# Kernel optimization log

Hardware: AMD Instinct MI355X
Metric: run time of the kernel (lower is better)

Reference implementation:

```python
import jax, jax.numpy as jnp
import numpy as np

H = 8          # heads
V = 25         # num_nodes
C_IN = 64      # node_channel_in
C_OUT = 64     # node_channel_out
M_IN = 64      # node_memory_in
N, T = 32, 256 # batch, time (t must equal mt)
DIN = V * C_IN     # 1600
DMEM = V * M_IN    # 1600
DOUT = V * C_OUT   # 1600


def setup_inputs() -> dict:
    key = jax.random.key(0)
    ks = jax.random.split(key, 8)
    s_in = 1.0 / np.sqrt(DIN)
    s_mem = 1.0 / np.sqrt(DMEM)
    return {
        "x": jax.random.normal(ks[0], (N, C_IN, T, V), jnp.float32),
        "m": jax.random.normal(ks[1], (N, M_IN, T, V), jnp.float32),
        # stacked per-head Linear weights, stored as [h, in, out]
        "Wk": jax.random.uniform(ks[2], (H, DIN, DOUT), jnp.float32, -s_in, s_in),
        "bk": jax.random.uniform(ks[3], (H, DOUT), jnp.float32, -s_in, s_in),
        "Wq": jax.random.uniform(ks[4], (H, DMEM, DOUT), jnp.float32, -s_mem, s_mem),
        "bq": jax.random.uniform(ks[5], (H, DOUT), jnp.float32, -s_mem, s_mem),
        "Wv": jax.random.uniform(ks[6], (H, DMEM, DOUT), jnp.float32, -s_mem, s_mem),
        "bv": jax.random.uniform(ks[7], (H, DOUT), jnp.float32, -s_mem, s_mem),
    }


def reference(x, m, Wk, bk, Wq, bq, Wv, bv):
    n, c, t, v = x.shape
    # [n,c,t,v] -> [n,t,c*v]
    xf = jnp.transpose(x, (0, 2, 1, 3)).reshape(n, t, c * v)
    mn, mc, mt, mv = m.shape
    mf = jnp.transpose(m, (0, 2, 1, 3)).reshape(mn, mt, mc * mv)
    # batched per-head projections: [n,h,t,dout]
    keys = jnp.einsum('ntf,hfo->nhto', xf, Wk) + bk[None, :, None, :]
    queries = jnp.einsum('ntf,hfo->nhto', mf, Wq) + bq[None, :, None, :]
    values = jnp.einsum('ntf,hfo->nhto', mf, Wv) + bv[None, :, None, :]
    scale = 1.0 / np.sqrt(C_OUT * V).astype(np.float32)
    # att: [n,h,mt,t]
    att = jnp.einsum('nhqd,nhkd->nhqk', queries, keys) * scale
    # NOTE: original applies softmax over dim=1 (the HEADS axis)
    att = jax.nn.softmax(att, axis=1)
    # [n,h,mt,t] @ [n,h,t(=mt),dout] -> [n,h,t,dout]
    y = jnp.einsum('nhqk,nhkd->nhqd', att, values)
    # [n,h,t,v*out] -> [n,t,v*out,h] -> [n,t,v,out*h] -> [n,out*h,t,v]
    y = jnp.transpose(y, (0, 2, 3, 1)).reshape(n, t, V, C_OUT * H)
    return jnp.transpose(y, (0, 3, 1, 2))
```

## Files before the change

### kernel.cpp

```cpp
#include <hip/hip_runtime.h>
#include <hip/hip_bf16.h>
#include <cstdint>

typedef __hip_bfloat16 bf16;
typedef __attribute__((ext_vector_type(8))) short short8;
typedef __attribute__((ext_vector_type(4))) float floatx4;

#define AS1 __attribute__((address_space(1)))
#define AS3 __attribute__((address_space(3)))

__device__ __forceinline__ int imin(int a, int b) { return a < b ? a : b; }

__device__ __forceinline__ void async_copy16(const void* g, void* l) {
  __builtin_amdgcn_global_load_lds((const AS1 uint32_t*)g, (AS3 uint32_t*)l, 16, 0, 0);
}

__global__ __launch_bounds__(256) void transpose_w(const float* __restrict__ W,
                                                   bf16* __restrict__ Wt) {
  __shared__ float tile[64][65];
  const float* Wh = W + (size_t)blockIdx.z * 2560000;
  bf16* Wth = Wt + (size_t)blockIdx.z * 2560000;
  const int i0 = blockIdx.x * 64;
  const int o0 = blockIdx.y * 64;
  for (int e = threadIdx.x; e < 4096; e += 256) {
    int r = e >> 6, c = e & 63;
    tile[r][c] = Wh[(size_t)(i0 + r) * 1600 + o0 + c];
  }
  __syncthreads();
  for (int e = threadIdx.x; e < 4096; e += 256) {
    int r = e >> 6, c = e & 63;
    Wth[(size_t)(o0 + r) * 1600 + i0 + c] = __float2bfloat16(tile[c][r]);
  }
}

__global__ __launch_bounds__(256) void pack_x(const float* __restrict__ X,
                                              bf16* __restrict__ Xf) {
  __shared__ float tile[32 * 200];
  const int n = blockIdx.z, tb = blockIdx.y * 8, cb = blockIdx.x * 32;
  const float* Xn = X + (size_t)n * 64 * 6400;
  for (int e = threadIdx.x; e < 6400; e += 256) {
    int c = e / 200, rv = e % 200;
    tile[e] = Xn[(size_t)(cb + c) * 6400 + tb * 25 + rv];
  }
  __syncthreads();
  bf16* dst = Xf + ((size_t)n * 256 + tb) * 1600 + cb * 25;
  for (int e = threadIdx.x; e < 6400; e += 256) {
    int t = e / 800, j = e % 800;
    int c = j / 25, v = j % 25;
    dst[(size_t)t * 1600 + j] = __float2bfloat16(tile[c * 200 + t * 25 + v]);
  }
}

template <int MODE>
__global__ __launch_bounds__(256) void gemm_bt(const short* __restrict__ Abase,
                                               const short* __restrict__ Bbase,
                                               const float* __restrict__ biasBase,
                                               void* __restrict__ outBase) {
  constexpr int M = (MODE == 0) ? 8192 : (MODE == 1) ? 1600 : 256;
  constexpr int N = (MODE == 0) ? 1600 : (MODE == 1) ? 8192 : (MODE == 2) ? 256 : 1600;
  constexpr int K = (MODE == 3) ? 256 : 1600;

  const int z = blockIdx.z;
  const short* A;
  const short* B;
  const float* bias = nullptr;
  if constexpr (MODE == 0) { A = Abase; B = Bbase + (size_t)z * 2560000; bias = biasBase + z * 1600; }
  if constexpr (MODE == 1) { A = Abase + (size_t)z * 2560000; B = Bbase; bias = biasBase + z * 1600; }
  if constexpr (MODE == 2) { A = Abase + (size_t)z * 409600; B = Bbase + (size_t)z * 409600; }
  if constexpr (MODE == 3) { A = Abase + (size_t)z * 65536; B = Bbase + (size_t)z * 409600; }

  __shared__ short As[128 * 32];
  __shared__ short Bs[128 * 32];

  const int tid = threadIdx.x;
  const int lane = tid & 63;
  const int wv = tid >> 6;
  const int m0 = blockIdx.x * 128;
  const int n0 = blockIdx.y * 128;

  const int srow = wv * 32 + (lane >> 2);
  const int scol = (lane & 3) * 8;
  const short* Ag0 = A + (size_t)imin(m0 + srow, M - 1) * K + scol;
  const short* Ag1 = A + (size_t)imin(m0 + srow + 16, M - 1) * K + scol;
  const short* Bg0 = B + (size_t)imin(n0 + srow, N - 1) * K + scol;
  const short* Bg1 = B + (size_t)imin(n0 + srow + 16, N - 1) * K + scol;

  short* Asw = &As[wv * 1024];
  short* Bsw = &Bs[wv * 1024];

  const int fr = lane & 15;
  const int fk = (lane >> 4) * 8;
  const int wm = (wv & 1) * 64;
  const int wn = (wv >> 1) * 64;

  floatx4 acc[4][4] = {};

  for (int k = 0; k < K; k += 32) {
    async_copy16(Ag0 + k, Asw);
    async_copy16(Ag1 + k, Asw + 512);
    async_copy16(Bg0 + k, Bsw);
    async_copy16(Bg1 + k, Bsw + 512);
    __syncthreads();
    short8 af[4], bfr[4];
#pragma unroll
    for (int i = 0; i < 4; i++) af[i] = *(const short8*)&As[(wm + i * 16 + fr) * 32 + fk];
#pragma unroll
    for (int j = 0; j < 4; j++) bfr[j] = *(const short8*)&Bs[(wn + j * 16 + fr) * 32 + fk];
#pragma unroll
    for (int i = 0; i < 4; i++)
#pragma unroll
      for (int j = 0; j < 4; j++)
        acc[i][j] = __builtin_amdgcn_mfma_f32_16x16x32_bf16(af[i], bfr[j], acc[i][j], 0, 0, 0);
    __syncthreads();
  }

  const int q4 = (lane >> 4) * 4;
#pragma unroll
  for (int i = 0; i < 4; i++) {
#pragma unroll
    for (int j = 0; j < 4; j++) {
#pragma unroll
      for (int r = 0; r < 4; r++) {
        const int mm = m0 + wm + i * 16 + q4 + r;
        const int nn = n0 + wn + j * 16 + fr;
        float v = acc[i][j][r];
        if constexpr (MODE == 0) {
          if (nn < 1600) {
            v += bias[nn];
            const int nb = mm >> 8, t = mm & 255;
            ((bf16*)outBase)[(((size_t)nb * 8 + z) * 256 + t) * 1600 + nn] = __float2bfloat16(v);
          }
        } else if constexpr (MODE == 1) {
          if (mm < 1600) {
            v += bias[mm];
            const int nb = nn >> 8, t = nn & 255;
            ((bf16*)outBase)[(((size_t)nb * 8 + z) * 1600 + mm) * 256 + t] = __float2bfloat16(v);
          }
        } else if constexpr (MODE == 2) {
          ((float*)outBase)[((size_t)z * 256 + mm) * 256 + nn] = v * 0.025f;
        } else {
          if (nn < 1600)
            ((bf16*)outBase)[((size_t)z * 256 + mm) * 1600 + nn] = __float2bfloat16(v);
        }
      }
    }
  }
}

__global__ __launch_bounds__(256) void softmax_h(const float* __restrict__ att,
                                                 bf16* __restrict__ P) {
  const size_t idx = (size_t)blockIdx.x * 256 + threadIdx.x;
  const int n = (int)(idx >> 16);
  const int rem = (int)(idx & 65535);
  const float* a = att + (size_t)n * 8 * 65536 + rem;
  float v[8];
  float mx = -1e30f;
#pragma unroll
  for (int h = 0; h < 8; h++) {
    v[h] = a[(size_t)h * 65536];
    mx = fmaxf(mx, v[h]);
  }
  float s = 0.f;
#pragma unroll
  for (int h = 0; h < 8; h++) {
    v[h] = __expf(v[h] - mx);
    s += v[h];
  }
  const float inv = 1.f / s;
  bf16* p = P + (size_t)n * 8 * 65536 + rem;
#pragma unroll
  for (int h = 0; h < 8; h++) p[(size_t)h * 65536] = __float2bfloat16(v[h] * inv);
}

__global__ __launch_bounds__(256) void unpack_y(const bf16* __restrict__ Y,
                                                float* __restrict__ out) {
  __shared__ bf16 tile[8 * 1600];
  const int tb = blockIdx.x * 8, h = blockIdx.y, n = blockIdx.z;
  const uint32_t* src = (const uint32_t*)(Y + (((size_t)n * 8 + h) * 256 + tb) * 1600);
  uint32_t* td = (uint32_t*)tile;
  for (int e = threadIdx.x; e < 6400; e += 256) td[e] = src[e];
  __syncthreads();
  for (int r = threadIdx.x; r < 512; r += 256) {
    const int c = r >> 3, t = r & 7;
    float* o = out + (((size_t)n * 512 + c * 8 + h) * 256 + tb + t) * 25;
    const bf16* s = tile + t * 1600 + c;
#pragma unroll
    for (int v = 0; v < 25; v++) o[v] = __bfloat162float(s[v * 64]);
  }
}

extern "C" void kernel_launch(void* const* d_in, const int* in_sizes, int n_in,
                              void* d_out, int out_size, void* d_ws, size_t ws_size,
                              hipStream_t stream) {
  const float* x = (const float*)d_in[0];
  const float* m = (const float*)d_in[1];
  const float* Wk = (const float*)d_in[2];
  const float* bk = (const float*)d_in[3];
  const float* Wq = (const float*)d_in[4];
  const float* bq = (const float*)d_in[5];
  const float* Wv = (const float*)d_in[6];
  const float* bv = (const float*)d_in[7];
  float* out = (float*)d_out;

  char* ws = (char*)d_ws;
  bf16* wkt = (bf16*)(ws);
  bf16* wqt = (bf16*)(ws + 40960000ll);
  bf16* wvt = (bf16*)(ws + 81920000ll);
  bf16* xf = (bf16*)(ws + 122880000ll);
  bf16* mf = (bf16*)(ws + 149094400ll);
  bf16* Kb = (bf16*)(ws + 175308800ll);
  bf16* Qb = (bf16*)(ws + 385024000ll);
  bf16* Vt = (bf16*)(ws + 594739200ll);
  float* att = (float*)(ws);
  bf16* P = (bf16*)(ws + 67108864ll);
  bf16* Yb = Qb;

  transpose_w<<<dim3(25, 25, 8), 256, 0, stream>>>(Wk, wkt);
  transpose_w<<<dim3(25, 25, 8), 256, 0, stream>>>(Wq, wqt);
  transpose_w<<<dim3(25, 25, 8), 256, 0, stream>>>(Wv, wvt);
  pack_x<<<dim3(2, 32, 32), 256, 0, stream>>>(x, xf);
  pack_x<<<dim3(2, 32, 32), 256, 0, stream>>>(m, mf);

  gemm_bt<0><<<dim3(64, 13, 8), 256, 0, stream>>>((const short*)xf, (const short*)wkt, bk, Kb);
  gemm_bt<0><<<dim3(64, 13, 8), 256, 0, stream>>>((const short*)mf, (const short*)wqt, bq, Qb);
  gemm_bt<1><<<dim3(13, 64, 8), 256, 0, stream>>>((const short*)wvt, (const short*)mf, bv, Vt);

  gemm_bt<2><<<dim3(2, 2, 256), 256, 0, stream>>>((const short*)Qb, (const short*)Kb, nullptr, att);
  softmax_h<<<dim3(8192), 256, 0, stream>>>(att, P);
  gemm_bt<3><<<dim3(2, 13, 256), 256, 0, stream>>>((const short*)P, (const short*)Vt, nullptr, Yb);

  unpack_y<<<dim3(32, 8, 32), 256, 0, stream>>>(Yb, out);
}
```

Measured before the change: 2.568 ms.

## Replace GEMMs with 256x256-tile double-buffered swizzled MFMA kernel

Replaces the 128x128 single-buffer GEMM with a 512-thread 256x256 tile kernel. It uses double-buffered LDS with async global-to-LDS prefetch of the next K slice, XOR-swizzled LDS layout to avoid bank conflicts, and phased MFMA scheduling with setprio. The per-head projections are merged into one wide GEMM (N=12800 / M=12800) instead of z-batched launches, and per-tile epilogue addressing is simplified. This raises reuse and overlaps loads with compute. The cost is heavy LDS use (128KB per block) and coarser tiles that waste work on edge tiles (e.g. the 1600-wide output in mode 3).

```diff
diff --git a/kernel.cpp b/kernel.cpp
--- a/kernel.cpp
+++ b/kernel.cpp
@@ -51,96 +51,154 @@
   }
 }
 
-template <int MODE>
-__global__ __launch_bounds__(256) void gemm_bt(const short* __restrict__ Abase,
-                                               const short* __restrict__ Bbase,
-                                               const float* __restrict__ biasBase,
-                                               void* __restrict__ outBase) {
-  constexpr int M = (MODE == 0) ? 8192 : (MODE == 1) ? 1600 : 256;
-  constexpr int N = (MODE == 0) ? 1600 : (MODE == 1) ? 8192 : (MODE == 2) ? 256 : 1600;
-  constexpr int K = (MODE == 3) ? 256 : 1600;
-
-  const int z = blockIdx.z;
-  const short* A;
-  const short* B;
-  const float* bias = nullptr;
-  if constexpr (MODE == 0) { A = Abase; B = Bbase + (size_t)z * 2560000; bias = biasBase + z * 1600; }
-  if constexpr (MODE == 1) { A = Abase + (size_t)z * 2560000; B = Bbase; bias = biasBase + z * 1600; }
-  if constexpr (MODE == 2) { A = Abase + (size_t)z * 409600; B = Bbase + (size_t)z * 409600; }
-  if constexpr (MODE == 3) { A = Abase + (size_t)z * 65536; B = Bbase + (size_t)z * 409600; }
-
-  __shared__ short As[128 * 32];
-  __shared__ short Bs[128 * 32];
-
-  const int tid = threadIdx.x;
+template <int FMODE>
+__global__ __launch_bounds__(512, 2) void gemm256(const short* __restrict__ Abase,
+                                                  const short* __restrict__ Bbase,
+                                                  const float* __restrict__ biasBase,
+                                                  void* __restrict__ outBase) {
+  constexpr int N = (FMODE == 0) ? 12800 : (FMODE == 1) ? 8192 : (FMODE == 2) ? 256 : 1600;
+  constexpr int K = (FMODE == 3) ? 256 : 1600;
+  constexpr int NT = K / 64;
+
+  __shared__ short As[2][256 * 64];
+  __shared__ short Bs[2][256 * 64];
+
+  const int tid = (int)threadIdx.x;
   const int lane = tid & 63;
   const int wv = tid >> 6;
-  const int m0 = blockIdx.x * 128;
-  const int n0 = blockIdx.y * 128;
-
-  const int srow = wv * 32 + (lane >> 2);
-  const int scol = (lane & 3) * 8;
-  const short* Ag0 = A + (size_t)imin(m0 + srow, M - 1) * K + scol;
-  const short* Ag1 = A + (size_t)imin(m0 + srow + 16, M - 1) * K + scol;
-  const short* Bg0 = B + (size_t)imin(n0 + srow, N - 1) * K + scol;
-  const short* Bg1 = B + (size_t)imin(n0 + srow + 16, N - 1) * K + scol;
-
-  short* Asw = &As[wv * 1024];
-  short* Bsw = &Bs[wv * 1024];
+  const int wr = wv >> 2;
+  const int wc = wv & 3;
+
+  const int z = blockIdx.z;
+  const short* A = Abase;
+  const short* B = Bbase;
+  if constexpr (FMODE == 2) { A += (size_t)z * 409600; B += (size_t)z * 409600; }
+  if constexpr (FMODE == 3) { A += (size_t)z * 65536;  B += (size_t)z * 409600; }
+
+  const int m0 = blockIdx.x * 256;
+  const int n0 = blockIdx.y * 256;
+
+  const int lr = lane >> 3;
+  const int lc = lane & 7;
+  const int sg8 = (lc ^ lr) * 8;
+
+  const short* AgI[4];
+  const short* BgI[4];
+#pragma unroll
+  for (int i = 0; i < 4; i++) {
+    const int ra = m0 + wv * 32 + i * 8 + lr;
+    int rb = n0 + wv * 32 + i * 8 + lr;
+    if constexpr (FMODE == 3) rb = imin(rb, N - 1);
+    AgI[i] = A + (size_t)ra * K + sg8;
+    BgI[i] = B + (size_t)rb * K + sg8;
+  }
 
   const int fr = lane & 15;
-  const int fk = (lane >> 4) * 8;
-  const int wm = (wv & 1) * 64;
-  const int wn = (wv >> 1) * 64;
-
-  floatx4 acc[4][4] = {};
-
-  for (int k = 0; k < K; k += 32) {
-    async_copy16(Ag0 + k, Asw);
-    async_copy16(Ag1 + k, Asw + 512);
-    async_copy16(Bg0 + k, Bsw);
-    async_copy16(Bg1 + k, Bsw + 512);
-    __syncthreads();
-    short8 af[4], bfr[4];
-#pragma unroll
-    for (int i = 0; i < 4; i++) af[i] = *(const short8*)&As[(wm + i * 16 + fr) * 32 + fk];
-#pragma unroll
-    for (int j = 0; j < 4; j++) bfr[j] = *(const short8*)&Bs[(wn + j * 16 + fr) * 32 + fk];
-#pragma unroll
-    for (int i = 0; i < 4; i++)
-#pragma unroll
-      for (int j = 0; j < 4; j++)
-        acc[i][j] = __builtin_amdgcn_mfma_f32_16x16x32_bf16(af[i], bfr[j], acc[i][j], 0, 0, 0);
-    __syncthreads();
-  }
-
-  const int q4 = (lane >> 4) * 4;
-#pragma unroll
-  for (int i = 0; i < 4; i++) {
+  const int fq = lane >> 4;
+  const int fr7 = fr & 7;
+  int swz[2];
+#pragma unroll
+  for (int ks = 0; ks < 2; ks++) swz[ks] = ((ks * 4 + fq) ^ fr7) * 8;
+
+  floatx4 acc[8][4] = {};
+  short8 af[4][2];
+  short8 bfrg[2][2];
+
+#define STAGE_A(bb, k0)                                                     \
+  { _Pragma("unroll") for (int i = 0; i < 4; i++)                           \
+      async_copy16(AgI[i] + (k0), &As[bb][(wv * 32 + i * 8) * 64]); }
+#define STAGE_B(bb, k0)                                                     \
+  { _Pragma("unroll") for (int i = 0; i < 4; i++)                           \
+      async_copy16(BgI[i] + (k0), &Bs[bb][(wv * 32 + i * 8) * 64]); }
+
+#define GPHASE(MQ, NQ, LOADA, STAGEC, ENDC)                                            \
+  {                                                                                    \
+    if constexpr (LOADA) {                                                             \
+      _Pragma("unroll") for (int mi = 0; mi < 4; mi++)                                 \
+          _Pragma("unroll") for (int ks = 0; ks < 2; ks++)                             \
+              af[mi][ks] = *(const short8*)&As[cur][(wr * 128 + MQ * 64 + mi * 16 + fr) * 64 + swz[ks]]; \
+    }                                                                                  \
+    _Pragma("unroll") for (int j = 0; j < 2; j++)                                      \
+        _Pragma("unroll") for (int ks = 0; ks < 2; ks++)                               \
+            bfrg[j][ks] = *(const short8*)&Bs[cur][(wc * 64 + NQ * 32 + j * 16 + fr) * 64 + swz[ks]]; \
+    STAGEC                                                                             \
+    __builtin_amdgcn_s_barrier();                                                      \
+    asm volatile("s_waitcnt lgkmcnt(0)" ::: "memory");                                 \
+    __builtin_amdgcn_sched_barrier(0);                                                 \
+    __builtin_amdgcn_s_setprio(1);                                                     \
+    _Pragma("unroll") for (int ks = 0; ks < 2; ks++)                                   \
+        _Pragma("unroll") for (int mi = 0; mi < 4; mi++)                               \
+            _Pragma("unroll") for (int j = 0; j < 2; j++)                              \
+                acc[MQ * 4 + mi][NQ * 2 + j] = __builtin_amdgcn_mfma_f32_16x16x32_bf16( \
+                    af[mi][ks], bfrg[j][ks], acc[MQ * 4 + mi][NQ * 2 + j], 0, 0, 0);   \
+    __builtin_amdgcn_s_setprio(0);                                                     \
+    ENDC                                                                               \
+    __builtin_amdgcn_s_barrier();                                                      \
+  }
+
+  STAGE_A(0, 0)
+  STAGE_B(0, 0)
+  asm volatile("s_waitcnt vmcnt(0)" ::: "memory");
+  __builtin_amdgcn_s_barrier();
+
+  int cur = 0;
+  for (int t = 0; t < NT; ++t) {
+    const int kn = (t + 1) * 64;
+    const bool pf = (t + 1 < NT);
+    const int nxt = cur ^ 1;
+    GPHASE(0, 0, true,  if (pf) STAGE_A(nxt, kn), )
+    GPHASE(0, 1, false, if (pf) STAGE_B(nxt, kn), )
+    GPHASE(1, 0, true,  , )
+    GPHASE(1, 1, false, , asm volatile("s_waitcnt vmcnt(0)" ::: "memory");)
+    cur = nxt;
+  }
+#undef GPHASE
+#undef STAGE_A
+#undef STAGE_B
+
+  const int q4 = fq * 4;
+#pragma unroll
+  for (int mi = 0; mi < 8; mi++) {
+    const int mmB = m0 + wr * 128 + mi * 16 + q4;
+    int h1 = 0, d1 = 0;
+    if constexpr (FMODE == 1) {
+      const int mb = m0 + wr * 128 + mi * 16;
+      h1 = mb / 1600;
+      d1 = mb - h1 * 1600 + q4;
+    }
 #pragma unroll
     for (int j = 0; j < 4; j++) {
-#pragma unroll
-      for (int r = 0; r < 4; r++) {
-        const int mm = m0 + wm + i * 16 + q4 + r;
-        const int nn = n0 + wn + j * 16 + fr;
-        float v = acc[i][j][r];
-        if constexpr (MODE == 0) {
-          if (nn < 1600) {
-            v += bias[nn];
-            const int nb = mm >> 8, t = mm & 255;
-            ((bf16*)outBase)[(((size_t)nb * 8 + z) * 256 + t) * 1600 + nn] = __float2bfloat16(v);
-          }
-        } else if constexpr (MODE == 1) {
-          if (mm < 1600) {
-            v += bias[mm];
-            const int nb = nn >> 8, t = nn & 255;
-            ((bf16*)outBase)[(((size_t)nb * 8 + z) * 1600 + mm) * 256 + t] = __float2bfloat16(v);
-          }
-        } else if constexpr (MODE == 2) {
-          ((float*)outBase)[((size_t)z * 256 + mm) * 256 + nn] = v * 0.025f;
-        } else {
-          if (nn < 1600)
-            ((bf16*)outBase)[((size_t)z * 256 + mm) * 1600 + nn] = __float2bfloat16(v);
+      const int nnb = n0 + wc * 64 + j * 16;
+      if constexpr (FMODE == 0) {
+        const int h = nnb / 1600;
+        const int d = nnb - h * 1600 + fr;
+        const float bv_ = biasBase[nnb + fr];
+#pragma unroll
+        for (int r = 0; r < 4; r++) {
+          const int mmr = mmB + r;
+          const int nb = mmr >> 8, tt = mmr & 255;
+          ((bf16*)outBase)[(((size_t)nb * 8 + h) * 256 + tt) * 1600 + d] =
+              __float2bfloat16(acc[mi][j][r] + bv_);
+        }
+      } else if constexpr (FMODE == 1) {
+        const int nn = nnb + fr;
+        const int nb = nn >> 8, tt = nn & 255;
+#pragma unroll
+        for (int r = 0; r < 4; r++) {
+          ((bf16*)outBase)[(((size_t)nb * 8 + h1) * 1600 + (d1 + r)) * 256 + tt] =
+              __float2bfloat16(acc[mi][j][r] + biasBase[mmB + r]);
+        }
+      } else if constexpr (FMODE == 2) {
+#pragma unroll
+        for (int r = 0; r < 4; r++)
+          ((float*)outBase)[((size_t)z * 256 + mmB + r) * 256 + nnb + fr] =
+              acc[mi][j][r] * 0.025f;
+      } else {
+        if (nnb < 1600) {
+#pragma unroll
+          for (int r = 0; r < 4; r++)
+            ((bf16*)outBase)[((size_t)z * 256 + mmB + r) * 1600 + nnb + fr] =
+                __float2bfloat16(acc[mi][j][r]);
         }
       }
     }
@@ -221,13 +279,13 @@
   pack_x<<<dim3(2, 32, 32), 256, 0, stream>>>(x, xf);
   pack_x<<<dim3(2, 32, 32), 256, 0, stream>>>(m, mf);
 
-  gemm_bt<0><<<dim3(64, 13, 8), 256, 0, stream>>>((const short*)xf, (const short*)wkt, bk, Kb);
-  gemm_bt<0><<<dim3(64, 13, 8), 256, 0, stream>>>((const short*)mf, (const short*)wqt, bq, Qb);
-  gemm_bt<1><<<dim3(13, 64, 8), 256, 0, stream>>>((const short*)wvt, (const short*)mf, bv, Vt);
-
-  gemm_bt<2><<<dim3(2, 2, 256), 256, 0, stream>>>((const short*)Qb, (const short*)Kb, nullptr, att);
+  gemm256<0><<<dim3(32, 50), 512, 0, stream>>>((const short*)xf, (const short*)wkt, bk, Kb);
+  gemm256<0><<<dim3(32, 50), 512, 0, stream>>>((const short*)mf, (const short*)wqt, bq, Qb);
+  gemm256<1><<<dim3(50, 32), 512, 0, stream>>>((const short*)wvt, (const short*)mf, bv, Vt);
+
+  gemm256<2><<<dim3(1, 1, 256), 512, 0, stream>>>((const short*)Qb, (const short*)Kb, nullptr, att);
   softmax_h<<<dim3(8192), 256, 0, stream>>>(att, P);
-  gemm_bt<3><<<dim3(2, 13, 256), 256, 0, stream>>>((const short*)P, (const short*)Vt, nullptr, Yb);
+  gemm256<3><<<dim3(1, 7, 256), 512, 0, stream>>>((const short*)P, (const short*)Vt, nullptr, Yb);
 
   unpack_y<<<dim3(32, 8, 32), 256, 0, stream>>>(Yb, out);
 }
```

New measurement: 2.276 ms. 1.13x faster.
